# Optimization experiments

Hardware: AMD Instinct MI355X
Metric: run time of the kernel (lower is better)

## Reference

```python
import jax, jax.numpy as jnp
import numpy as np

N_QUBITS = 12
FAST_DEPTH = 4
FAST_DECAY = 0.9
LATENT = 512
BATCH = 2048


def _apply_ry(state, theta, wire):
    # state: (B, 2**n) real; RY is a real rotation. PennyLane default.qubit:
    # wire 0 is the most-significant bit of the state index.
    B = state.shape[0]
    s = state.reshape(B, 1 << wire, 2, -1)
    h = theta * 0.5
    c = jnp.cos(h)[:, None, None]
    sn = jnp.sin(h)[:, None, None]
    s0, s1 = s[:, :, 0], s[:, :, 1]
    out = jnp.stack([c * s0 - sn * s1, sn * s0 + c * s1], axis=2)
    return out.reshape(state.shape)


def _apply_cnot_adjacent(state, wire):
    # CNOT with control=wire, target=wire+1 (nearest-neighbor chain)
    B = state.shape[0]
    s = state.reshape(B, 1 << wire, 2, 2, -1)
    out = jnp.stack([s[:, :, 0], s[:, :, 1, ::-1]], axis=2)
    return out.reshape(state.shape)


def _fwp_circuit(x, fast, n_qubits, n_outputs):
    # x: (B, n_qubits) RY encoding angles; fast: (B, depth, n_qubits)
    B = x.shape[0]
    dim = 1 << n_qubits
    # Hadamard layer on |0...0> -> uniform positive real amplitudes.
    state = jnp.full((B, dim), 2.0 ** (-n_qubits / 2), dtype=x.dtype)
    for w in range(n_qubits):
        state = _apply_ry(state, x[:, w], w)
    for layer in range(fast.shape[1]):
        for w in range(n_qubits - 1):
            state = _apply_cnot_adjacent(state, w)
        for w in range(n_qubits):
            state = _apply_ry(state, fast[:, layer, w], w)
    probs = state * state  # real state -> |amp|^2
    outs = []
    for w in range(n_outputs):
        p = probs.reshape(B, 1 << w, 2, -1)
        outs.append(p[:, :, 0].sum(axis=(1, 2)) - p[:, :, 1].sum(axis=(1, 2)))
    return jnp.stack(outs, axis=1)  # (B, n_outputs) PauliZ expvals


def setup_inputs() -> dict:
    key = jax.random.key(0)
    ks = jax.random.split(key, 6)
    n, depth, latent = N_QUBITS, FAST_DEPTH, LATENT
    return {
        "x_t": jax.random.normal(ks[0], (BATCH, n), jnp.float32),
        "fast_prev": jax.random.normal(ks[1], (BATCH, depth, n), jnp.float32) * 0.1,
        "W_enc": jax.random.normal(ks[2], (latent, n), jnp.float32) / np.sqrt(n).astype(np.float32),
        "b_enc": jnp.zeros((latent,), jnp.float32),
        "W_upd": jax.random.normal(ks[3], (depth * n, latent), jnp.float32) / np.sqrt(latent).astype(np.float32),
        "b_upd": jnp.zeros((depth * n,), jnp.float32),
        "W_ro": jax.random.normal(ks[4], (1, n), jnp.float32) / np.sqrt(n).astype(np.float32),
        "b_ro": jnp.zeros((1,), jnp.float32),
    }


def reference(x_t, fast_prev, W_enc, b_enc, W_upd, b_upd, W_ro, b_ro):
    latent = jnp.tanh(x_t @ W_enc.T + b_enc)
    delta = (latent @ W_upd.T + b_upd).reshape(x_t.shape[0], FAST_DEPTH, N_QUBITS)
    fast_next = FAST_DECAY * fast_prev + delta
    q_out = _fwp_circuit(x_t, fast_next, N_QUBITS, N_QUBITS)  # n_outputs = n_qubits
    y_t = q_out @ W_ro.T + b_ro
    return (y_t, fast_next)
```

## Files before the change

kernel.cpp:

```cpp
#include <hip/hip_runtime.h>

static constexpr int NQ    = 12;
static constexpr int DEPTH = 4;
static constexpr int LAT   = 512;
static constexpr int FAST  = DEPTH * NQ;
static constexpr float DECAY = 0.9f;
static constexpr int PITCH = 66;

using v2f = __attribute__((ext_vector_type(2))) float;


template<int S, int B>
__device__ __forceinline__ void bfly_half(float (&v)[64], float c, float s) {
    v2f c2 = {c, c}, s2 = {s, s};
    #pragma unroll
    for (int r0 = B; r0 < B + 32; r0 += 2) {
        if ((r0 & S) == 0) {
            v2f a = {v[r0],     v[r0 + 1]};
            v2f b = {v[r0 + S], v[r0 + S + 1]};
            v2f na = c2 * a - s2 * b;
            v2f nb = s2 * a + c2 * b;
            v[r0]     = na.x;  v[r0 + 1]     = na.y;
            v[r0 + S] = nb.x;  v[r0 + S + 1] = nb.y;
        }
    }
}

template<int B>
__device__ __forceinline__ void bfly1_half(float (&v)[64], float c, float s) {
    v2f cs = {c, s}, nsc = {-s, c};
    #pragma unroll
    for (int r0 = B; r0 < B + 32; r0 += 2) {
        float a = v[r0], b = v[r0 + 1];
        v2f aa = {a, a}, bb = {b, b};
        v2f res = cs * aa + nsc * bb;
        v[r0]     = res.x;
        v[r0 + 1] = res.y;
    }
}

template<int B>
__device__ __forceinline__ void ry5_half(float (&v)[64], const float* c, const float* s) {
    bfly_half<16, B>(v, c[0], s[0]);
    bfly_half<8,  B>(v, c[1], s[1]);
    bfly_half<4,  B>(v, c[2], s[2]);
    bfly_half<2,  B>(v, c[3], s[3]);
    bfly1_half<B>(v, c[4], s[4]);
}

__device__ __forceinline__ void bfly32(float (&v)[64], float c, float s) {
    v2f c2 = {c, c}, s2 = {s, s};
    #pragma unroll
    for (int r0 = 0; r0 < 32; r0 += 2) {
        v2f a = {v[r0],      v[r0 + 1]};
        v2f b = {v[r0 + 32], v[r0 + 33]};
        v2f na = c2 * a - s2 * b;
        v2f nb = s2 * a + c2 * b;
        v[r0]      = na.x;  v[r0 + 1]  = na.y;
        v[r0 + 32] = nb.x;  v[r0 + 33] = nb.y;
    }
}

__device__ __forceinline__ void xw(const float (&v)[64], float* s_xch, int lane) {
    #pragma unroll
    for (int k = 0; k < 32; k++)
        *(v2f*)&s_xch[lane * PITCH + 2 * k] = (v2f){v[2 * k], v[2 * k + 1]};
}

__device__ __forceinline__ void p1r(float (&v)[64], const float* s_xch, int A0, int A1) {
    #pragma unroll
    for (int r = 0; r < 64; r++) {
        const int g = r ^ (r >> 1);
        v[r] = s_xch[g * PITCH + ((r & 1) ? A1 : A0)];
    }
}

__device__ __forceinline__ void p2r(float (&v)[64], const float* s_xch, int lane) {
    #pragma unroll
    for (int r = 0; r < 64; r++) v[r] = s_xch[r * PITCH + lane];
}

__device__ __forceinline__ void init_state(float (&v)[64], const float (&xa)[NQ], int lane) {
    float g0[NQ], g1[NQ];
    #pragma unroll
    for (int w = 0; w < NQ; w++) {
        float hh = 0.5f * xa[w];
        float c = __cosf(hh), s = __sinf(hh);
        g0[w] = (c - s) * 0.70710678118654752f;
        g1[w] = (c + s) * 0.70710678118654752f;
    }
    float L = 1.0f;
    #pragma unroll
    for (int w = 0; w < 6; w++)
        L *= ((lane >> (5 - w)) & 1) ? g1[w] : g0[w];
    v[0] = L;
    #pragma unroll
    for (int w = 6; w < NQ; w++) {
        const int S = 1 << (11 - w);
        #pragma unroll
        for (int r = 0; r < 64; r += 2 * S) {
            v[r + S] = v[r] * g1[w];
            v[r]     = v[r] * g0[w];
        }
    }
}

__global__ __launch_bounds__(64, 1)
void fwp_kernel(const float* __restrict__ x_t,
                const float* __restrict__ fast_prev,
                const float* __restrict__ W_enc,
                const float* __restrict__ b_enc,
                const float* __restrict__ W_upd,
                const float* __restrict__ b_upd,
                const float* __restrict__ W_ro,
                const float* __restrict__ b_ro,
                float* __restrict__ out_y,
                float* __restrict__ out_fast) {
    const int lane = threadIdx.x;
    const int eA   = 2 * blockIdx.x;
    const int eB   = eA + 1;

    __shared__ __align__(16) float s_xch[64 * PITCH];
    __shared__ __align__(8)  float s_csA[2 * FAST], s_csB[2 * FAST];

    float* s_latA = s_xch;
    float* s_latB = s_xch + LAT;

    float xaA[NQ], xaB[NQ];
    #pragma unroll
    for (int k = 0; k < NQ; k++) {
        xaA[k] = x_t[eA * NQ + k];
        xaB[k] = x_t[eB * NQ + k];
    }

    #pragma unroll
    for (int t = 0; t < LAT / 64; t++) {
        int j = lane + 64 * t;
        const float4* wr = (const float4*)(W_enc + j * NQ);
        float4 a0 = wr[0], a1 = wr[1], a2 = wr[2];
        float be = b_enc[j];
        float sA = be
            + a0.x * xaA[0] + a0.y * xaA[1] + a0.z * xaA[2]  + a0.w * xaA[3]
            + a1.x * xaA[4] + a1.y * xaA[5] + a1.z * xaA[6]  + a1.w * xaA[7]
            + a2.x * xaA[8] + a2.y * xaA[9] + a2.z * xaA[10] + a2.w * xaA[11];
        float sB = be
            + a0.x * xaB[0] + a0.y * xaB[1] + a0.z * xaB[2]  + a0.w * xaB[3]
            + a1.x * xaB[4] + a1.y * xaB[5] + a1.z * xaB[6]  + a1.w * xaB[7]
            + a2.x * xaB[8] + a2.y * xaB[9] + a2.z * xaB[10] + a2.w * xaB[11];
        s_latA[j] = tanhf(sA);
        s_latB[j] = tanhf(sB);
    }

    if (lane < FAST) {
        const float4* wr = (const float4*)(W_upd + lane * LAT);
        const float4* la = (const float4*)(s_latA);
        const float4* lb = (const float4*)(s_latB);
        float sA = b_upd[lane], sB = sA;
        #pragma unroll 8
        for (int j = 0; j < LAT / 4; j++) {
            float4 w4 = wr[j];
            float4 a4 = la[j];
            float4 b4 = lb[j];
            sA += w4.x * a4.x + w4.y * a4.y + w4.z * a4.z + w4.w * a4.w;
            sB += w4.x * b4.x + w4.y * b4.y + w4.z * b4.z + w4.w * b4.w;
        }
        float angA = DECAY * fast_prev[eA * FAST + lane] + sA;
        float angB = DECAY * fast_prev[eB * FAST + lane] + sB;
        out_fast[eA * FAST + lane] = angA;
        out_fast[eB * FAST + lane] = angB;
        *(v2f*)&s_csA[2 * lane] = (v2f){__cosf(0.5f * angA), __sinf(0.5f * angA)};
        *(v2f*)&s_csB[2 * lane] = (v2f){__cosf(0.5f * angB), __sinf(0.5f * angB)};
    }

    float vA[64], vB[64];
    init_state(vA, xaA, lane);
    init_state(vB, xaB, lane);

    const int A0 = ((lane ^ (lane >> 1)) & 31) | (lane & 32);
    const int A1 = A0 ^ 32;

    #pragma unroll 1
    for (int layer = 0; layer < DEPTH; layer++) {
        float lcA[NQ], lsA[NQ], lcB[NQ], lsB[NQ];
        #pragma unroll
        for (int w = 0; w < NQ; w++) {
            v2f ca = *(const v2f*)&s_csA[2 * (layer * NQ + w)];
            v2f cb = *(const v2f*)&s_csB[2 * (layer * NQ + w)];
            lcA[w] = ca.x;  lsA[w] = ca.y;
            lcB[w] = cb.x;  lsB[w] = cb.y;
        }

        xw(vA, s_xch, lane);
        p1r(vA, s_xch, A0, A1);
        xw(vB, s_xch, lane);
        ry5_half<0>(vA, lcA + 1, lsA + 1);
        p1r(vB, s_xch, A0, A1);
        ry5_half<32>(vA, lcA + 1, lsA + 1);
        bfly32(vA, lcA[0], lsA[0]);
        ry5_half<0>(vB, lcB + 1, lsB + 1);

        xw(vA, s_xch, lane);
        ry5_half<32>(vB, lcB + 1, lsB + 1);
        bfly32(vB, lcB[0], lsB[0]);
        p2r(vA, s_xch, lane);
        xw(vB, s_xch, lane);
        ry5_half<0>(vA, lcA + 7, lsA + 7);
        p2r(vB, s_xch, lane);
        ry5_half<32>(vA, lcA + 7, lsA + 7);
        bfly32(vA, lcA[6], lsA[6]);
        ry5_half<0>(vB, lcB + 7, lsB + 7);
        ry5_half<32>(vB, lcB + 7, lsB + 7);
        bfly32(vB, lcB[6], lsB[6]);
    }

    float wro[NQ];
    #pragma unroll
    for (int w = 0; w < NQ; w++) wro[w] = W_ro[w];
    float sl = 0.0f;
    #pragma unroll
    for (int w = 0; w < 6; w++)
        sl += ((lane >> (5 - w)) & 1) ? -wro[w] : wro[w];

    float totA = 0.0f, pwA[6] = {0,0,0,0,0,0};
    float totB = 0.0f, pwB[6] = {0,0,0,0,0,0};
    #pragma unroll
    for (int r = 0; r < 64; r++) {
        float pA = vA[r] * vA[r];
        float pB = vB[r] * vB[r];
        totA += pA;  totB += pB;
        pwA[0] += (r & 32) ? -pA : pA;  pwB[0] += (r & 32) ? -pB : pB;
        pwA[1] += (r & 16) ? -pA : pA;  pwB[1] += (r & 16) ? -pB : pB;
        pwA[2] += (r & 8)  ? -pA : pA;  pwB[2] += (r & 8)  ? -pB : pB;
        pwA[3] += (r & 4)  ? -pA : pA;  pwB[3] += (r & 4)  ? -pB : pB;
        pwA[4] += (r & 2)  ? -pA : pA;  pwB[4] += (r & 2)  ? -pB : pB;
        pwA[5] += (r & 1)  ? -pA : pA;  pwB[5] += (r & 1)  ? -pB : pB;
    }
    float yA = sl * totA, yB = sl * totB;
    #pragma unroll
    for (int k = 0; k < 6; k++) {
        yA += wro[6 + k] * pwA[k];
        yB += wro[6 + k] * pwB[k];
    }
    #pragma unroll
    for (int m = 32; m >= 1; m >>= 1) {
        yA += __shfl_xor(yA, m, 64);
        yB += __shfl_xor(yB, m, 64);
    }
    if (lane == 0) {
        float br = b_ro[0];
        out_y[eA] = yA + br;
        out_y[eB] = yB + br;
    }
}

extern "C" void kernel_launch(void* const* d_in, const int* in_sizes, int n_in,
                              void* d_out, int out_size, void* d_ws, size_t ws_size,
                              hipStream_t stream) {
    const float* x_t       = (const float*)d_in[0];
    const float* fast_prev = (const float*)d_in[1];
    const float* W_enc     = (const float*)d_in[2];
    const float* b_enc     = (const float*)d_in[3];
    const float* W_upd     = (const float*)d_in[4];
    const float* b_upd     = (const float*)d_in[5];
    const float* W_ro      = (const float*)d_in[6];
    const float* b_ro      = (const float*)d_in[7];
    float* out = (float*)d_out;

    fwp_kernel<<<1024, 64, 0, stream>>>(x_t, fast_prev, W_enc, b_enc,
                                        W_upd, b_upd, W_ro, b_ro,
                                        out , out + 2048 );
}
```

Measured before the change: 108.3 us.

## Use separate per-state LDS exchange buffers with float4 transposes and pitch 68

Gives each of the two statevectors its own shared-memory exchange buffer, so the interleaved A/B schedule is replaced by a simpler sequential one. The padded row pitch goes from 66 to 68 so rows can be moved with 128-bit float4 stores and loads. The second transpose now writes column-wise and reads rows as float4 instead of writing rows and reading columns. The encoder also gives each lane 8 contiguous latent rows so it can load and store them as float4. This doubles LDS use per block and drops the overlap of one state's compute with the other's exchange, and the new access patterns may cause different bank conflicts.

```diff
diff --git a/kernel.cpp b/kernel.cpp
--- a/kernel.cpp
+++ b/kernel.cpp
@@ -5,7 +5,7 @@
 static constexpr int LAT   = 512;
 static constexpr int FAST  = DEPTH * NQ;
 static constexpr float DECAY = 0.9f;
-static constexpr int PITCH = 66;
+static constexpr int P     = 68;
 
 using v2f = __attribute__((ext_vector_type(2))) float;
 
@@ -40,12 +40,12 @@
 }
 
 template<int B>
-__device__ __forceinline__ void ry5_half(float (&v)[64], const float* c, const float* s) {
-    bfly_half<16, B>(v, c[0], s[0]);
-    bfly_half<8,  B>(v, c[1], s[1]);
-    bfly_half<4,  B>(v, c[2], s[2]);
-    bfly_half<2,  B>(v, c[3], s[3]);
-    bfly1_half<B>(v, c[4], s[4]);
+__device__ __forceinline__ void ry5_half(float (&v)[64], const v2f* cs) {
+    bfly_half<16, B>(v, cs[0].x, cs[0].y);
+    bfly_half<8,  B>(v, cs[1].x, cs[1].y);
+    bfly_half<4,  B>(v, cs[2].x, cs[2].y);
+    bfly_half<2,  B>(v, cs[3].x, cs[3].y);
+    bfly1_half<B>(v, cs[4].x, cs[4].y);
 }
 
 __device__ __forceinline__ void bfly32(float (&v)[64], float c, float s) {
@@ -61,23 +61,27 @@
     }
 }
 
-__device__ __forceinline__ void xw(const float (&v)[64], float* s_xch, int lane) {
-    #pragma unroll
-    for (int k = 0; k < 32; k++)
-        *(v2f*)&s_xch[lane * PITCH + 2 * k] = (v2f){v[2 * k], v[2 * k + 1]};
-}
-
-__device__ __forceinline__ void p1r(float (&v)[64], const float* s_xch, int A0, int A1) {
+__device__ __forceinline__ void pass1(float (&v)[64], float* X, int lane, int A0, int A1) {
+    #pragma unroll
+    for (int k = 0; k < 16; k++)
+        *(float4*)&X[lane * P + 4 * k] =
+            (float4){v[4 * k], v[4 * k + 1], v[4 * k + 2], v[4 * k + 3]};
     #pragma unroll
     for (int r = 0; r < 64; r++) {
         const int g = r ^ (r >> 1);
-        v[r] = s_xch[g * PITCH + ((r & 1) ? A1 : A0)];
-    }
-}
-
-__device__ __forceinline__ void p2r(float (&v)[64], const float* s_xch, int lane) {
-    #pragma unroll
-    for (int r = 0; r < 64; r++) v[r] = s_xch[r * PITCH + lane];
+        v[r] = X[g * P + ((r & 1) ? A1 : A0)];
+    }
+}
+
+__device__ __forceinline__ void pass2(float (&v)[64], float* X, int lane) {
+    #pragma unroll
+    for (int q = 0; q < 64; q++) X[q * P + lane] = v[q];
+    #pragma unroll
+    for (int k = 0; k < 16; k++) {
+        float4 t = *(const float4*)&X[lane * P + 4 * k];
+        v[4 * k]     = t.x;  v[4 * k + 1] = t.y;
+        v[4 * k + 2] = t.z;  v[4 * k + 3] = t.w;
+    }
 }
 
 __device__ __forceinline__ void init_state(float (&v)[64], const float (&xa)[NQ], int lane) {
@@ -120,11 +124,12 @@
     const int eA   = 2 * blockIdx.x;
     const int eB   = eA + 1;
 
-    __shared__ __align__(16) float s_xch[64 * PITCH];
-    __shared__ __align__(8)  float s_csA[2 * FAST], s_csB[2 * FAST];
-
-    float* s_latA = s_xch;
-    float* s_latB = s_xch + LAT;
+    __shared__ __align__(16) float XA[64 * P];
+    __shared__ __align__(16) float XB[64 * P];
+    __shared__ __align__(8)  v2f   csA[FAST], csB[FAST];
+
+    float* latA = XA;
+    float* latB = XB;
 
     float xaA[NQ], xaB[NQ];
     #pragma unroll
@@ -133,29 +138,38 @@
         xaB[k] = x_t[eB * NQ + k];
     }
 
-    #pragma unroll
-    for (int t = 0; t < LAT / 64; t++) {
-        int j = lane + 64 * t;
-        const float4* wr = (const float4*)(W_enc + j * NQ);
-        float4 a0 = wr[0], a1 = wr[1], a2 = wr[2];
-        float be = b_enc[j];
-        float sA = be
-            + a0.x * xaA[0] + a0.y * xaA[1] + a0.z * xaA[2]  + a0.w * xaA[3]
-            + a1.x * xaA[4] + a1.y * xaA[5] + a1.z * xaA[6]  + a1.w * xaA[7]
-            + a2.x * xaA[8] + a2.y * xaA[9] + a2.z * xaA[10] + a2.w * xaA[11];
-        float sB = be
-            + a0.x * xaB[0] + a0.y * xaB[1] + a0.z * xaB[2]  + a0.w * xaB[3]
-            + a1.x * xaB[4] + a1.y * xaB[5] + a1.z * xaB[6]  + a1.w * xaB[7]
-            + a2.x * xaB[8] + a2.y * xaB[9] + a2.z * xaB[10] + a2.w * xaB[11];
-        s_latA[j] = tanhf(sA);
-        s_latB[j] = tanhf(sB);
+    {
+        const float4* we = (const float4*)(W_enc + lane * 8 * NQ);
+        float4 be0 = *(const float4*)&b_enc[8 * lane];
+        float4 be1 = *(const float4*)&b_enc[8 * lane + 4];
+        float be[8] = {be0.x, be0.y, be0.z, be0.w, be1.x, be1.y, be1.z, be1.w};
+        float lA[8], lB[8];
+        #pragma unroll
+        for (int t = 0; t < 8; t++) {
+            float4 a0 = we[3 * t], a1 = we[3 * t + 1], a2 = we[3 * t + 2];
+            float sA = be[t]
+                + a0.x * xaA[0] + a0.y * xaA[1] + a0.z * xaA[2]  + a0.w * xaA[3]
+                + a1.x * xaA[4] + a1.y * xaA[5] + a1.z * xaA[6]  + a1.w * xaA[7]
+                + a2.x * xaA[8] + a2.y * xaA[9] + a2.z * xaA[10] + a2.w * xaA[11];
+            float sB = be[t]
+                + a0.x * xaB[0] + a0.y * xaB[1] + a0.z * xaB[2]  + a0.w * xaB[3]
+                + a1.x * xaB[4] + a1.y * xaB[5] + a1.z * xaB[6]  + a1.w * xaB[7]
+                + a2.x * xaB[8] + a2.y * xaB[9] + a2.z * xaB[10] + a2.w * xaB[11];
+            lA[t] = tanhf(sA);
+            lB[t] = tanhf(sB);
+        }
+        *(float4*)&latA[8 * lane]     = (float4){lA[0], lA[1], lA[2], lA[3]};
+        *(float4*)&latA[8 * lane + 4] = (float4){lA[4], lA[5], lA[6], lA[7]};
+        *(float4*)&latB[8 * lane]     = (float4){lB[0], lB[1], lB[2], lB[3]};
+        *(float4*)&latB[8 * lane + 4] = (float4){lB[4], lB[5], lB[6], lB[7]};
     }
 
     if (lane < FAST) {
         const float4* wr = (const float4*)(W_upd + lane * LAT);
-        const float4* la = (const float4*)(s_latA);
-        const float4* lb = (const float4*)(s_latB);
-        float sA = b_upd[lane], sB = sA;
+        const float4* la = (const float4*)(latA);
+        const float4* lb = (const float4*)(latB);
+        float base = b_upd[lane];
+        float sA = base, sB = base;
         #pragma unroll 8
         for (int j = 0; j < LAT / 4; j++) {
             float4 w4 = wr[j];
@@ -168,8 +182,8 @@
         float angB = DECAY * fast_prev[eB * FAST + lane] + sB;
         out_fast[eA * FAST + lane] = angA;
         out_fast[eB * FAST + lane] = angB;
-        *(v2f*)&s_csA[2 * lane] = (v2f){__cosf(0.5f * angA), __sinf(0.5f * angA)};
-        *(v2f*)&s_csB[2 * lane] = (v2f){__cosf(0.5f * angB), __sinf(0.5f * angB)};
+        csA[lane] = (v2f){__cosf(0.5f * angA), __sinf(0.5f * angA)};
+        csB[lane] = (v2f){__cosf(0.5f * angB), __sinf(0.5f * angB)};
     }
 
     float vA[64], vB[64];
@@ -181,36 +195,29 @@
 
     #pragma unroll 1
     for (int layer = 0; layer < DEPTH; layer++) {
-        float lcA[NQ], lsA[NQ], lcB[NQ], lsB[NQ];
+        v2f ca[NQ], cb[NQ];
         #pragma unroll
         for (int w = 0; w < NQ; w++) {
-            v2f ca = *(const v2f*)&s_csA[2 * (layer * NQ + w)];
-            v2f cb = *(const v2f*)&s_csB[2 * (layer * NQ + w)];
-            lcA[w] = ca.x;  lsA[w] = ca.y;
-            lcB[w] = cb.x;  lsB[w] = cb.y;
-        }
-
-        xw(vA, s_xch, lane);
-        p1r(vA, s_xch, A0, A1);
-        xw(vB, s_xch, lane);
-        ry5_half<0>(vA, lcA + 1, lsA + 1);
-        p1r(vB, s_xch, A0, A1);
-        ry5_half<32>(vA, lcA + 1, lsA + 1);
-        bfly32(vA, lcA[0], lsA[0]);
-        ry5_half<0>(vB, lcB + 1, lsB + 1);
-
-        xw(vA, s_xch, lane);
-        ry5_half<32>(vB, lcB + 1, lsB + 1);
-        bfly32(vB, lcB[0], lsB[0]);
-        p2r(vA, s_xch, lane);
-        xw(vB, s_xch, lane);
-        ry5_half<0>(vA, lcA + 7, lsA + 7);
-        p2r(vB, s_xch, lane);
-        ry5_half<32>(vA, lcA + 7, lsA + 7);
-        bfly32(vA, lcA[6], lsA[6]);
-        ry5_half<0>(vB, lcB + 7, lsB + 7);
-        ry5_half<32>(vB, lcB + 7, lsB + 7);
-        bfly32(vB, lcB[6], lsB[6]);
+            ca[w] = csA[layer * NQ + w];
+            cb[w] = csB[layer * NQ + w];
+        }
+
+        pass1(vA, XA, lane, A0, A1);
+        ry5_half<0>(vA, ca + 1);
+        ry5_half<32>(vA, ca + 1);
+        bfly32(vA, ca[0].x, ca[0].y);
+        pass1(vB, XB, lane, A0, A1);
+        ry5_half<0>(vB, cb + 1);
+        ry5_half<32>(vB, cb + 1);
+        bfly32(vB, cb[0].x, cb[0].y);
+        pass2(vA, XA, lane);
+        ry5_half<0>(vA, ca + 7);
+        ry5_half<32>(vA, ca + 7);
+        bfly32(vA, ca[6].x, ca[6].y);
+        pass2(vB, XB, lane);
+        ry5_half<0>(vB, cb + 7);
+        ry5_half<32>(vB, cb + 7);
+        bfly32(vB, cb[6].x, cb[6].y);
     }
 
     float wro[NQ];
```

Result: no change. 106.2 us (-1.9%).
